# Kernel tuning notes

Measured on AMD Instinct MI355X. Metric: run time of the kernel, lower is better.

## Reference

```python
import jax, jax.numpy as jnp
import numpy as np

N = 2708
IN_C = 1433
OUT_C = 64


def setup_inputs() -> dict:
    key = jax.random.key(0)
    k1, k2, k3, k4, k5, k6, k7 = jax.random.split(key, 7)
    X = jax.random.normal(k1, (N, IN_C), dtype=jnp.float32)
    A = jax.random.randint(k2, (N, N), 0, 2, dtype=jnp.int32)  # dense binary adjacency mask
    # Graph Fourier basis: orthonormal-ish random matrix (QR of gaussian)
    U = jnp.linalg.qr(jax.random.normal(k3, (N, N), dtype=jnp.float32))[0]
    s = 1.0 / np.sqrt(IN_C)
    W_K = jax.random.normal(k4, (OUT_C, IN_C), dtype=jnp.float32) * s
    W_Q = jax.random.normal(k5, (OUT_C, IN_C), dtype=jnp.float32) * s
    W_V = jax.random.normal(k6, (OUT_C, IN_C), dtype=jnp.float32) * s
    lmbd = jax.random.uniform(k7, (N, 1), dtype=jnp.float32)
    return {"X": X, "A": A, "U": U, "W_K": W_K, "W_Q": W_Q, "W_V": W_V, "lmbd": lmbd}


def reference(X, A, U, W_K, W_Q, W_V, lmbd):
    # Linear projections (torch nn.Linear: x @ W.T)
    K = X @ W_K.T  # [N, d]
    Q = X @ W_Q.T  # [N, d]
    V = X @ W_V.T  # [N, d]
    d_k = K.shape[-1]
    E = (Q @ K.T) / d_k  # [N, N]
    # spectral filtering: igft(lmbd * gft(E)) = U @ (lmbd * (U^T @ E))
    E = jnp.abs(U @ (lmbd * (U.T @ E)))
    # masked softmax over neighbors; dropout p=0 in eval mode (no-op)
    E_masked = jnp.where(A == 0, -jnp.inf, E)
    alpha = jax.nn.softmax(E_masked, axis=-1)
    H = alpha @ V  # [N, d]
    return H
```

## Files before the change

kernel.cpp:

```cpp
#include <hip/hip_runtime.h>

#define NV 2708
#define INC 1433
#define XCOLS 1472
#define UDIM 2752
#define PSTR 2728
#define BSTR 2752
#define SLAB ((size_t)(2752*64))
#define MWPR 88
#define NSP 8
#define NSU 22

typedef __attribute__((ext_vector_type(8))) short bf16x8;
typedef __attribute__((ext_vector_type(4))) float f32x4;
typedef __attribute__((ext_vector_type(4))) unsigned short u16x4;

__device__ __forceinline__ unsigned short f2bf(float f){
  union { float f; unsigned int i; } v; v.f = f;
  return (unsigned short)((v.i + 0x7fffu + ((v.i >> 16) & 1u)) >> 16);
}

__device__ __forceinline__ void conv_row(const float* __restrict__ src,
                                         unsigned short* __restrict__ dst, int tid){
  const int sh = ((unsigned int)((size_t)src >> 2)) & 1;
  if (tid == 0){ int ce = sh ? 0 : (INC - 1); dst[ce] = f2bf(src[ce]); }
  const float2* s2 = (const float2*)(src + sh);
  for (int c2 = tid; c2 < (INC - 1)/2; c2 += 256){
    float2 v = s2[c2];
    int c = sh + c2*2;
    dst[c]     = f2bf(v.x);
    dst[c + 1] = f2bf(v.y);
  }
  for (int c = INC + tid; c < XCOLS; c += 256) dst[c] = 0;
}

__global__ __launch_bounds__(256) void convert_all(
    const float* __restrict__ X, const float* __restrict__ WK,
    const float* __restrict__ WQ, const float* __restrict__ WV,
    const float* __restrict__ U, const int* __restrict__ A,
    unsigned short* __restrict__ Xbf, unsigned short* __restrict__ Wbf,
    unsigned short* __restrict__ Ubf, unsigned int* __restrict__ Abits)
{
  const int bx = blockIdx.x;
  const int tid = threadIdx.x;
  if (bx < 2752){
    const int row = bx;
    unsigned short* dst = Ubf + (size_t)row*UDIM;
    if (row < NV){
      const float* src = U + (size_t)row*NV;
      for (int c4 = tid; c4 < 688; c4 += 256){
        float4 v = make_float4(0.f,0.f,0.f,0.f);
        if (c4 < 677) v = *(const float4*)(src + c4*4);
        u16x4 h = { f2bf(v.x), f2bf(v.y), f2bf(v.z), f2bf(v.w) };
        *(u16x4*)(dst + c4*4) = h;
      }
    } else {
      u16x4 zz = {0,0,0,0};
      for (int c4 = tid; c4 < 688; c4 += 256) *(u16x4*)(dst + c4*4) = zz;
    }
  } else if (bx < 5504){
    const int row = bx - 2752;
    unsigned short* dst = Xbf + (size_t)row*XCOLS;
    if (row < NV){
      conv_row(X + (size_t)row*INC, dst, tid);
    } else {
      u16x4 zz = {0,0,0,0};
      for (int c4 = tid; c4 < XCOLS/4; c4 += 256) *(u16x4*)(dst + c4*4) = zz;
    }
  } else if (bx < 5696){
    const int row = bx - 5504;
    const float* s = (row < 64) ? WK : (row < 128) ? WQ : WV;
    conv_row(s + (size_t)(row & 63)*INC, Wbf + (size_t)row*XCOLS, tid);
  } else {
    const int i = bx - 5696;
    const int lane = tid & 63, wave = tid >> 6;
    const int* arow = A + (size_t)i*NV;
    unsigned int* drow = Abits + (size_t)i*MWPR;
    for (int g = wave; g < 11; g += 4){
      int base = g*256 + lane*4;
      int4 v = make_int4(0,0,0,0);
      if (base < NV) v = *(const int4*)(arow + base);
      unsigned long long m0 = __ballot(v.x != 0);
      unsigned long long m1 = __ballot(v.y != 0);
      unsigned long long m2 = __ballot(v.z != 0);
      unsigned long long m3 = __ballot(v.w != 0);
      if (lane < 8){
        unsigned long long mm = (lane < 2) ? m0 : (lane < 4) ? m1 : (lane < 6) ? m2 : m3;
        drow[g*8 + lane] = (lane & 1) ? (unsigned int)(mm >> 32) : (unsigned int)mm;
      }
    }
  }
}

__global__ __launch_bounds__(256) void proj(
    const unsigned short* __restrict__ Xbf, const unsigned short* __restrict__ Wbf,
    float* __restrict__ part)
{
  __shared__ __align__(16) unsigned short At[64*72];
  __shared__ __align__(16) unsigned short Bt[64*72];
  const int tid = threadIdx.x;
  const int lane = tid & 63, wave = tid >> 6, quad = lane >> 4, lr = lane & 15;
  const int m0 = blockIdx.x * 64;
  const int s  = blockIdx.y, z = blockIdx.z;
  const int kbeg = s * 192, kend = min(kbeg + 192, XCOLS);
  const int wm = (wave & 1) * 32, wn = (wave >> 1) * 32;
  const unsigned short* Wz = Wbf + (size_t)z*64*XCOLS;
  const int srow = wave*8 + (lane >> 3), seg = lane & 7;
  f32x4 acc[2][2] = {};

  for (int k0 = kbeg; k0 < kend; k0 += 64){
    #pragma unroll
    for (int e = 0; e < 2; e++){
      int row = e*32 + srow;
      bf16x8 xa = *(const bf16x8*)(Xbf + (size_t)(m0+row)*XCOLS + k0 + seg*8);
      bf16x8 wb = *(const bf16x8*)(Wz  + (size_t)row*XCOLS      + k0 + seg*8);
      *(bf16x8*)&At[row*72 + seg*8] = xa;
      *(bf16x8*)&Bt[row*72 + seg*8] = wb;
    }
    __syncthreads();
    #pragma unroll
    for (int ks = 0; ks < 2; ks++){
      bf16x8 af[2], bv[2];
      #pragma unroll
      for (int t = 0; t < 2; t++){
        af[t] = *(const bf16x8*)&At[(wm + t*16 + lr)*72 + ks*32 + quad*8];
        bv[t] = *(const bf16x8*)&Bt[(wn + t*16 + lr)*72 + ks*32 + quad*8];
      }
      #pragma unroll
      for (int tm = 0; tm < 2; tm++)
        #pragma unroll
        for (int tn = 0; tn < 2; tn++)
          acc[tm][tn] = __builtin_amdgcn_mfma_f32_16x16x32_bf16(af[tm], bv[tn], acc[tm][tn], 0, 0, 0);
    }
    __syncthreads();
  }
  float* dst = part + (size_t)(z*NSP + s) * SLAB;
  #pragma unroll
  for (int tm = 0; tm < 2; tm++)
    #pragma unroll
    for (int tn = 0; tn < 2; tn++)
      #pragma unroll
      for (int e = 0; e < 4; e++)
        dst[(size_t)(m0 + wm + tm*16 + quad*4 + e)*64 + wn + tn*16 + lr] = acc[tm][tn][e];
}

__global__ __launch_bounds__(256) void reduce_proj(
    const float* __restrict__ part, unsigned short* __restrict__ K16f,
    unsigned short* __restrict__ QT16, unsigned short* __restrict__ VTf)
{
  int idx = blockIdx.x*256 + threadIdx.x;
  int z = blockIdx.y;
  int m = idx >> 6, c = idx & 63;
  const float* base = part + (size_t)z*NSP*SLAB + idx;
  float v = 0.f;
  #pragma unroll
  for (int s = 0; s < NSP; s++) v += base[s*SLAB];
  unsigned short h = (m < NV) ? f2bf(v) : (unsigned short)0;
  if (z == 0){
    if (m < 2720) K16f[((m>>4)*2 + (c>>5))*512 + (m&15)*32 + (c&31)] = h;
  } else if (z == 1){
    QT16[(size_t)c*BSTR + m] = h;
  } else {
    if (m < 2720) VTf[(m>>5)*2048 + c*32 + (m&31)] = h;
  }
}

__global__ __launch_bounds__(256) void gemmG(
    const unsigned short* __restrict__ Ubf, const unsigned short* __restrict__ QT,
    float* __restrict__ part)
{
  __shared__ __align__(16) unsigned short At[64*72];
  __shared__ __align__(16) unsigned short Bt[64*72];
  const int tid = threadIdx.x;
  const int lane = tid & 63, wave = tid >> 6, quad = lane >> 4, lr = lane & 15;
  const int m0 = blockIdx.x * 64;
  const int s  = blockIdx.y;
  const int kbeg = s * 128, kend = min(kbeg + 128, UDIM);
  const int wm = (wave & 1) * 32, wn = (wave >> 1) * 32;
  const int bc = tid >> 2, bseg = tid & 3;
  const int ml = (lane & 15)*4, koff = wave*16 + (lane >> 4);
  f32x4 acc[2][2] = {};

  for (int k0 = kbeg; k0 < kend; k0 += 64){
    #pragma unroll
    for (int e = 0; e < 4; e++){
      int kl = koff + e*4;
      u16x4 v = *(const u16x4*)(Ubf + (size_t)(k0+kl)*UDIM + m0 + ml);
      At[(ml+0)*72 + kl] = v[0];
      At[(ml+1)*72 + kl] = v[1];
      At[(ml+2)*72 + kl] = v[2];
      At[(ml+3)*72 + kl] = v[3];
    }
    {
      const unsigned short* q = QT + (size_t)bc*BSTR + k0 + bseg*16;
      *(bf16x8*)&Bt[bc*72 + bseg*16]     = *(const bf16x8*)(q);
      *(bf16x8*)&Bt[bc*72 + bseg*16 + 8] = *(const bf16x8*)(q + 8);
    }
    __syncthreads();
    #pragma unroll
    for (int ks = 0; ks < 2; ks++){
      bf16x8 af[2], bv[2];
      #pragma unroll
      for (int t = 0; t < 2; t++){
        af[t] = *(const bf16x8*)&At[(wm + t*16 + lr)*72 + ks*32 + quad*8];
        bv[t] = *(const bf16x8*)&Bt[(wn + t*16 + lr)*72 + ks*32 + quad*8];
      }
      #pragma unroll
      for (int tm = 0; tm < 2; tm++)
        #pragma unroll
        for (int tn = 0; tn < 2; tn++)
          acc[tm][tn] = __builtin_amdgcn_mfma_f32_16x16x32_bf16(af[tm], bv[tn], acc[tm][tn], 0, 0, 0);
    }
    __syncthreads();
  }
  float* dst = part + (size_t)s * SLAB;
  #pragma unroll
  for (int tm = 0; tm < 2; tm++)
    #pragma unroll
    for (int tn = 0; tn < 2; tn++)
      #pragma unroll
      for (int e = 0; e < 4; e++)
        dst[(size_t)(m0 + wm + tm*16 + quad*4 + e)*64 + wn + tn*16 + lr] = acc[tm][tn][e];
}

__global__ __launch_bounds__(256) void reduce_g(
    const float* __restrict__ part, const float* __restrict__ lm,
    unsigned short* __restrict__ G2T)
{
  int idx = blockIdx.x*256 + threadIdx.x;
  int m = idx >> 6, c = idx & 63;
  const float* base = part + idx;
  float v = 0.f;
  #pragma unroll
  for (int s = 0; s < NSU; s++) v += base[s*SLAB];
  unsigned short h = 0;
  if (m < NV) h = f2bf(v * lm[m] * (1.0f/64.0f));
  G2T[(size_t)c*BSTR + m] = h;
}

__global__ __launch_bounds__(256) void gemmF(
    const unsigned short* __restrict__ Ubf, const unsigned short* __restrict__ G2T,
    float* __restrict__ part)
{
  __shared__ __align__(16) unsigned short At[64*72];
  __shared__ __align__(16) unsigned short Bt[64*72];
  const int tid = threadIdx.x;
  const int lane = tid & 63, wave = tid >> 6, quad = lane >> 4, lr = lane & 15;
  const int m0 = blockIdx.x * 64;
  const int s  = blockIdx.y;
  const int kbeg = s * 128, kend = min(kbeg + 128, UDIM);
  const int wm = (wave & 1) * 32, wn = (wave >> 1) * 32;
  const int bc = tid >> 2, bseg = tid & 3;
  const int srow = wave*8 + (lane >> 3), seg = lane & 7;
  f32x4 acc[2][2] = {};

  for (int k0 = kbeg; k0 < kend; k0 += 64){
    #pragma unroll
    for (int e = 0; e < 2; e++){
      int row = e*32 + srow;
      bf16x8 ua = *(const bf16x8*)(Ubf + (size_t)(m0+row)*UDIM + k0 + seg*8);
      *(bf16x8*)&At[row*72 + seg*8] = ua;
    }
    {
      const unsigned short* g = G2T + (size_t)bc*BSTR + k0 + bseg*16;
      *(bf16x8*)&Bt[bc*72 + bseg*16]     = *(const bf16x8*)(g);
      *(bf16x8*)&Bt[bc*72 + bseg*16 + 8] = *(const bf16x8*)(g + 8);
    }
    __syncthreads();
    #pragma unroll
    for (int ks = 0; ks < 2; ks++){
      bf16x8 af[2], bv[2];
      #pragma unroll
      for (int t = 0; t < 2; t++){
        af[t] = *(const bf16x8*)&At[(wm + t*16 + lr)*72 + ks*32 + quad*8];
        bv[t] = *(const bf16x8*)&Bt[(wn + t*16 + lr)*72 + ks*32 + quad*8];
      }
      #pragma unroll
      for (int tm = 0; tm < 2; tm++)
        #pragma unroll
        for (int tn = 0; tn < 2; tn++)
          acc[tm][tn] = __builtin_amdgcn_mfma_f32_16x16x32_bf16(af[tm], bv[tn], acc[tm][tn], 0, 0, 0);
    }
    __syncthreads();
  }
  float* dst = part + (size_t)s * SLAB;
  #pragma unroll
  for (int tm = 0; tm < 2; tm++)
    #pragma unroll
    for (int tn = 0; tn < 2; tn++)
      #pragma unroll
      for (int e = 0; e < 4; e++)
        dst[(size_t)(m0 + wm + tm*16 + quad*4 + e)*64 + wn + tn*16 + lr] = acc[tm][tn][e];
}

__global__ __launch_bounds__(512) void fused_attn(
    const float* __restrict__ partF, const unsigned short* __restrict__ K16f,
    const unsigned int* __restrict__ Abits, const unsigned short* __restrict__ VTf,
    float* __restrict__ Hout)
{
  __shared__ __align__(16) unsigned short pbuf[16*PSTR];
  __shared__ __align__(16) unsigned short fbuf[16*64];
  __shared__ unsigned int mrow[16*MWPR];
  __shared__ float swave[8][16];
  __shared__ float rinv[16];
  __shared__ __align__(16) float obuf[4][256];
  const int tid  = threadIdx.x;
  const int lane = tid & 63, wave = tid >> 6;
  const int quad = lane >> 4, lr = lane & 15;
  const int i0 = blockIdx.x * 16;

  #pragma unroll
  for (int h = 0; h < 2; h++){
    int idx = h*512 + tid;
    const float* base = partF + (size_t)(i0 + (idx >> 6))*64 + (idx & 63);
    float v = 0.f;
    #pragma unroll
    for (int s = 0; s < NSU; s++) v += base[s*SLAB];
    fbuf[idx] = f2bf(v);
  }
  for (int idx = tid; idx < 16*MWPR; idx += 512){
    int r = idx / MWPR;
    unsigned int v = 0;
    if (i0 + r < NV) v = Abits[(size_t)(i0 + r)*MWPR + (idx - r*MWPR)];
    mrow[idx] = v;
  }
  __syncthreads();

  const bf16x8 af0 = *(const bf16x8*)&fbuf[lr*64 + quad*8];
  const bf16x8 af1 = *(const bf16x8*)&fbuf[lr*64 + 32 + quad*8];
  float psum[4] = {0.f, 0.f, 0.f, 0.f};
  {
    int t = wave;
    const unsigned short* kb = K16f + t*1024 + lr*32 + quad*8;
    bf16x8 b0 = *(const bf16x8*)(kb);
    bf16x8 b1 = *(const bf16x8*)(kb + 512);
    while (t < 170){
      int tn = t + 8;
      bf16x8 n0 = b0, n1 = b1;
      if (tn < 170){
        const unsigned short* nb = K16f + tn*1024 + lr*32 + quad*8;
        n0 = *(const bf16x8*)(nb);
        n1 = *(const bf16x8*)(nb + 512);
      }
      f32x4 sv0 = {}, sv1 = {};
      sv0 = __builtin_amdgcn_mfma_f32_16x16x32_bf16(af0, b0, sv0, 0, 0, 0);
      sv1 = __builtin_amdgcn_mfma_f32_16x16x32_bf16(af1, b1, sv1, 0, 0, 0);
      f32x4 sv = sv0 + sv1;
      {
        int col = t*16 + lr;
        int ss = col & 255, ll = ss >> 2;
        int wsh = (col >> 8)*8 + (ss & 3)*2 + (ll >> 5);
        int bit = ll & 31;
        #pragma unroll
        for (int e = 0; e < 4; e++){
          int r = quad*4 + e;
          float p = 0.f;
          if ((mrow[r*MWPR + wsh] >> bit) & 1u) p = __expf(fabsf(sv[e]));
          psum[e] += p;
          pbuf[r*PSTR + col] = f2bf(p);
        }
      }
      b0 = n0; b1 = n1; t = tn;
    }
  }
  #pragma unroll
  for (int e = 0; e < 4; e++){
    float v = psum[e];
    #pragma unroll
    for (int o = 1; o <= 8; o <<= 1) v += __shfl_xor(v, o, 64);
    if (lr == 0) swave[wave][quad*4 + e] = v;
  }
  __syncthreads();
  if (tid < 16){
    float s = 0.f;
    #pragma unroll
    for (int w = 0; w < 8; w++) s += swave[w][tid];
    rinv[tid] = (s > 0.f) ? (1.f/s) : 0.f;
  }
  __syncthreads();

  const int c0 = (wave & 3) * 16;
  const int ktbeg = (wave >> 2) ? 43 : 0;
  const int ktend = (wave >> 2) ? 85 : 43;
  f32x4 acc = {};
  {
    bf16x8 bv = *(const bf16x8*)&VTf[ktbeg*2048 + (c0 + lr)*32 + quad*8];
    for (int kt = ktbeg; kt < ktend; kt++){
      bf16x8 bn = bv;
      if (kt + 1 < ktend) bn = *(const bf16x8*)&VTf[(kt+1)*2048 + (c0 + lr)*32 + quad*8];
      bf16x8 af = *(const bf16x8*)&pbuf[lr*PSTR + kt*32 + quad*8];
      acc = __builtin_amdgcn_mfma_f32_16x16x32_bf16(af, bv, acc, 0, 0, 0);
      bv = bn;
    }
  }
  if (wave >= 4) *(f32x4*)&obuf[wave & 3][lane*4] = acc;
  __syncthreads();
  if (wave < 4){
    f32x4 o = *(const f32x4*)&obuf[wave][lane*4];
    acc += o;
    #pragma unroll
    for (int e = 0; e < 4; e++){
      int r = quad*4 + e;
      int i = i0 + r;
      if (i < NV) Hout[(size_t)i*64 + c0 + lr] = acc[e] * rinv[r];
    }
  }
}

extern "C" void kernel_launch(void* const* d_in, const int* in_sizes, int n_in,
                              void* d_out, int out_size, void* d_ws, size_t ws_size,
                              hipStream_t stream){
  (void)in_sizes; (void)n_in; (void)out_size; (void)ws_size;
  const float* X  = (const float*)d_in[0];
  const int*   A  = (const int*)d_in[1];
  const float* U  = (const float*)d_in[2];
  const float* WK = (const float*)d_in[3];
  const float* WQ = (const float*)d_in[4];
  const float* WV = (const float*)d_in[5];
  const float* lm = (const float*)d_in[6];

  char* ws = (char*)d_ws;
  size_t off = 0;
  auto alloc = [&](size_t bytes){ size_t o = off; off = (off + bytes + 255) & ~(size_t)255; return o; };
  float*          part = (float*)(ws + alloc(24*SLAB*4));
  unsigned short* Ubf  = (unsigned short*)(ws + alloc((size_t)UDIM*UDIM*2));
  unsigned short* Xbf  = (unsigned short*)(ws + alloc((size_t)UDIM*XCOLS*2));
  unsigned short* Wbf  = (unsigned short*)(ws + alloc((size_t)192*XCOLS*2));
  unsigned short* K16f = (unsigned short*)(ws + alloc((size_t)170*1024*2));
  unsigned short* QT16 = (unsigned short*)(ws + alloc((size_t)64*BSTR*2));
  unsigned short* G2T  = (unsigned short*)(ws + alloc((size_t)64*BSTR*2));
  unsigned short* VTf  = (unsigned short*)(ws + alloc((size_t)85*2048*2));
  unsigned int*   Abits= (unsigned int*)(ws + alloc((size_t)NV*MWPR*4));

  convert_all<<<dim3(8404), 256, 0, stream>>>(X, WK, WQ, WV, U, A, Xbf, Wbf, Ubf, Abits);
  proj<<<dim3(43, NSP, 3), 256, 0, stream>>>(Xbf, Wbf, part);
  reduce_proj<<<dim3(688, 3), 256, 0, stream>>>(part, K16f, QT16, VTf);
  gemmG<<<dim3(43, NSU), 256, 0, stream>>>(Ubf, QT16, part);
  reduce_g<<<dim3(688), 256, 0, stream>>>(part, lm, G2T);
  gemmF<<<dim3(43, NSU), 256, 0, stream>>>(Ubf, G2T, part);
  fused_attn<<<dim3(170), 512, 0, stream>>>(part, K16f, Abits, VTf, (float*)d_out);
}
```

Measured before the change: 182.1 us.

## Replace split-K partial buffers and reduce kernels with atomic accumulation

```diff
diff --git a/kernel.cpp b/kernel.cpp
--- a/kernel.cpp
+++ b/kernel.cpp
@@ -6,10 +6,10 @@
 #define UDIM 2752
 #define PSTR 2728
 #define BSTR 2752
-#define SLAB ((size_t)(2752*64))
 #define MWPR 88
 #define NSP 8
 #define NSU 22
+#define ACCN 176128
 
 typedef __attribute__((ext_vector_type(8))) short bf16x8;
 typedef __attribute__((ext_vector_type(4))) float f32x4;
@@ -38,25 +38,34 @@
     const float* __restrict__ X, const float* __restrict__ WK,
     const float* __restrict__ WQ, const float* __restrict__ WV,
     const float* __restrict__ U, const int* __restrict__ A,
+    const float* __restrict__ lm,
     unsigned short* __restrict__ Xbf, unsigned short* __restrict__ Wbf,
-    unsigned short* __restrict__ Ubf, unsigned int* __restrict__ Abits)
+    unsigned short* __restrict__ Ubf, unsigned short* __restrict__ UbfL,
+    unsigned int* __restrict__ Abits, float* __restrict__ acc32)
 {
   const int bx = blockIdx.x;
   const int tid = threadIdx.x;
   if (bx < 2752){
     const int row = bx;
-    unsigned short* dst = Ubf + (size_t)row*UDIM;
+    unsigned short* dst  = Ubf  + (size_t)row*UDIM;
+    unsigned short* dstl = UbfL + (size_t)row*UDIM;
     if (row < NV){
       const float* src = U + (size_t)row*NV;
+      const float s = 1.0f/64.0f;
       for (int c4 = tid; c4 < 688; c4 += 256){
         float4 v = make_float4(0.f,0.f,0.f,0.f);
-        if (c4 < 677) v = *(const float4*)(src + c4*4);
-        u16x4 h = { f2bf(v.x), f2bf(v.y), f2bf(v.z), f2bf(v.w) };
-        *(u16x4*)(dst + c4*4) = h;
+        float4 l4 = make_float4(0.f,0.f,0.f,0.f);
+        if (c4 < 677){ v = *(const float4*)(src + c4*4); l4 = *(const float4*)(lm + c4*4); }
+        u16x4 h  = { f2bf(v.x), f2bf(v.y), f2bf(v.z), f2bf(v.w) };
+        u16x4 hl = { f2bf(v.x*l4.x*s), f2bf(v.y*l4.y*s), f2bf(v.z*l4.z*s), f2bf(v.w*l4.w*s) };
+        *(u16x4*)(dst  + c4*4) = h;
+        *(u16x4*)(dstl + c4*4) = hl;
       }
     } else {
       u16x4 zz = {0,0,0,0};
-      for (int c4 = tid; c4 < 688; c4 += 256) *(u16x4*)(dst + c4*4) = zz;
+      for (int c4 = tid; c4 < 688; c4 += 256){
+        *(u16x4*)(dst + c4*4) = zz; *(u16x4*)(dstl + c4*4) = zz;
+      }
     }
   } else if (bx < 5504){
     const int row = bx - 2752;
@@ -71,7 +80,7 @@
     const int row = bx - 5504;
     const float* s = (row < 64) ? WK : (row < 128) ? WQ : WV;
     conv_row(s + (size_t)(row & 63)*INC, Wbf + (size_t)row*XCOLS, tid);
-  } else {
+  } else if (bx < 8404){
     const int i = bx - 5696;
     const int lane = tid & 63, wave = tid >> 6;
     const int* arow = A + (size_t)i*NV;
@@ -89,12 +98,15 @@
         drow[g*8 + lane] = (lane & 1) ? (unsigned int)(mm >> 32) : (unsigned int)mm;
       }
     }
+  } else {
+    int idx = (bx - 8404)*256 + tid;
+    *(float4*)(acc32 + (size_t)idx*4) = make_float4(0.f,0.f,0.f,0.f);
   }
 }
 
 __global__ __launch_bounds__(256) void proj(
     const unsigned short* __restrict__ Xbf, const unsigned short* __restrict__ Wbf,
-    float* __restrict__ part)
+    float* __restrict__ K32, float* __restrict__ Q32, float* __restrict__ V32)
 {
   __shared__ __align__(16) unsigned short At[64*72];
   __shared__ __align__(16) unsigned short Bt[64*72];
@@ -134,40 +146,30 @@
     }
     __syncthreads();
   }
-  float* dst = part + (size_t)(z*NSP + s) * SLAB;
   #pragma unroll
   for (int tm = 0; tm < 2; tm++)
     #pragma unroll
     for (int tn = 0; tn < 2; tn++)
       #pragma unroll
-      for (int e = 0; e < 4; e++)
-        dst[(size_t)(m0 + wm + tm*16 + quad*4 + e)*64 + wn + tn*16 + lr] = acc[tm][tn][e];
-}
-
-__global__ __launch_bounds__(256) void reduce_proj(
-    const float* __restrict__ part, unsigned short* __restrict__ K16f,
-    unsigned short* __restrict__ QT16, unsigned short* __restrict__ VTf)
-{
-  int idx = blockIdx.x*256 + threadIdx.x;
-  int z = blockIdx.y;
-  int m = idx >> 6, c = idx & 63;
-  const float* base = part + (size_t)z*NSP*SLAB + idx;
-  float v = 0.f;
-  #pragma unroll
-  for (int s = 0; s < NSP; s++) v += base[s*SLAB];
-  unsigned short h = (m < NV) ? f2bf(v) : (unsigned short)0;
-  if (z == 0){
-    if (m < 2720) K16f[((m>>4)*2 + (c>>5))*512 + (m&15)*32 + (c&31)] = h;
-  } else if (z == 1){
-    QT16[(size_t)c*BSTR + m] = h;
-  } else {
-    if (m < 2720) VTf[(m>>5)*2048 + c*32 + (m&31)] = h;
-  }
+      for (int e = 0; e < 4; e++){
+        int m = m0 + wm + tm*16 + quad*4 + e;
+        int c = wn + tn*16 + lr;
+        float v = acc[tm][tn][e];
+        if (z == 0){
+          if (m < 2720) atomicAdd(&K32[((m>>4)*2 + (c>>5))*512 + (m&15)*32 + (c&31)], v);
+        } else if (z == 1){
+          atomicAdd(&Q32[(size_t)c*BSTR + m], v);
+        } else {
+          if (m < 2720) atomicAdd(&V32[(m>>5)*2048 + c*32 + (m&31)], v);
+        }
+      }
 }
 
 __global__ __launch_bounds__(256) void gemmG(
-    const unsigned short* __restrict__ Ubf, const unsigned short* __restrict__ QT,
-    float* __restrict__ part)
+    const unsigned short* __restrict__ UbfL, const float* __restrict__ Q32,
+    float* __restrict__ G32,
+    const float* __restrict__ K32, const float* __restrict__ V32,
+    unsigned short* __restrict__ K16f, unsigned short* __restrict__ VTf)
 {
   __shared__ __align__(16) unsigned short At[64*72];
   __shared__ __align__(16) unsigned short Bt[64*72];
@@ -181,20 +183,38 @@
   const int ml = (lane & 15)*4, koff = wave*16 + (lane >> 4);
   f32x4 acc[2][2] = {};
 
+  {
+    int bid = blockIdx.y*43 + blockIdx.x;
+    for (int i = bid*256 + tid; i < 2*174080; i += 946*256){
+      if (i < 174080) K16f[i] = f2bf(K32[i]);
+      else            VTf[i - 174080] = f2bf(V32[i - 174080]);
+    }
+  }
+
   for (int k0 = kbeg; k0 < kend; k0 += 64){
     #pragma unroll
     for (int e = 0; e < 4; e++){
       int kl = koff + e*4;
-      u16x4 v = *(const u16x4*)(Ubf + (size_t)(k0+kl)*UDIM + m0 + ml);
+      u16x4 v = *(const u16x4*)(UbfL + (size_t)(k0+kl)*UDIM + m0 + ml);
       At[(ml+0)*72 + kl] = v[0];
       At[(ml+1)*72 + kl] = v[1];
       At[(ml+2)*72 + kl] = v[2];
       At[(ml+3)*72 + kl] = v[3];
     }
     {
-      const unsigned short* q = QT + (size_t)bc*BSTR + k0 + bseg*16;
-      *(bf16x8*)&Bt[bc*72 + bseg*16]     = *(const bf16x8*)(q);
-      *(bf16x8*)&Bt[bc*72 + bseg*16 + 8] = *(const bf16x8*)(q + 8);
+      const float* q = Q32 + (size_t)bc*BSTR + k0 + bseg*16;
+      float4 qa = *(const float4*)(q);
+      float4 qb = *(const float4*)(q + 4);
+      float4 qc = *(const float4*)(q + 8);
+      float4 qd = *(const float4*)(q + 12);
+      u16x4 h0 = { f2bf(qa.x), f2bf(qa.y), f2bf(qa.z), f2bf(qa.w) };
+      u16x4 h1 = { f2bf(qb.x), f2bf(qb.y), f2bf(qb.z), f2bf(qb.w) };
+      u16x4 h2 = { f2bf(qc.x), f2bf(qc.y), f2bf(qc.z), f2bf(qc.w) };
+      u16x4 h3 = { f2bf(qd.x), f2bf(qd.y), f2bf(qd.z), f2bf(qd.w) };
+      *(u16x4*)&Bt[bc*72 + bseg*16]      = h0;
+      *(u16x4*)&Bt[bc*72 + bseg*16 + 4]  = h1;
+      *(u16x4*)&Bt[bc*72 + bseg*16 + 8]  = h2;
+      *(u16x4*)&Bt[bc*72 + bseg*16 + 12] = h3;
     }
     __syncthreads();
     #pragma unroll
@@ -213,34 +233,21 @@
     }
     __syncthreads();
   }
-  float* dst = part + (size_t)s * SLAB;
   #pragma unroll
   for (int tm = 0; tm < 2; tm++)
     #pragma unroll
     for (int tn = 0; tn < 2; tn++)
       #pragma unroll
-      for (int e = 0; e < 4; e++)
-        dst[(size_t)(m0 + wm + tm*16 + quad*4 + e)*64 + wn + tn*16 + lr] = acc[tm][tn][e];
-}
-
-__global__ __launch_bounds__(256) void reduce_g(
-    const float* __restrict__ part, const float* __restrict__ lm,
-    unsigned short* __restrict__ G2T)
-{
-  int idx = blockIdx.x*256 + threadIdx.x;
-  int m = idx >> 6, c = idx & 63;
-  const float* base = part + idx;
-  float v = 0.f;
-  #pragma unroll
-  for (int s = 0; s < NSU; s++) v += base[s*SLAB];
-  unsigned short h = 0;
-  if (m < NV) h = f2bf(v * lm[m] * (1.0f/64.0f));
-  G2T[(size_t)c*BSTR + m] = h;
+      for (int e = 0; e < 4; e++){
+        int m = m0 + wm + tm*16 + quad*4 + e;
+        int c = wn + tn*16 + lr;
+        atomicAdd(&G32[(size_t)c*BSTR + m], acc[tm][tn][e]);
+      }
 }
 
 __global__ __launch_bounds__(256) void gemmF(
-    const unsigned short* __restrict__ Ubf, const unsigned short* __restrict__ G2T,
-    float* __restrict__ part)
+    const unsigned short* __restrict__ Ubf, const float* __restrict__ G32,
+    float* __restrict__ F32)
 {
   __shared__ __align__(16) unsigned short At[64*72];
   __shared__ __align__(16) unsigned short Bt[64*72];
@@ -262,9 +269,19 @@
       *(bf16x8*)&At[row*72 + seg*8] = ua;
     }
     {
-      const unsigned short* g = G2T + (size_t)bc*BSTR + k0 + bseg*16;
-      *(bf16x8*)&Bt[bc*72 + bseg*16]     = *(const bf16x8*)(g);
-      *(bf16x8*)&Bt[bc*72 + bseg*16 + 8] = *(const bf16x8*)(g + 8);
+      const float* g = G32 + (size_t)bc*BSTR + k0 + bseg*16;
+      float4 qa = *(const float4*)(g);
+      float4 qb = *(const float4*)(g + 4);
+      float4 qc = *(const float4*)(g + 8);
+      float4 qd = *(const float4*)(g + 12);
+      u16x4 h0 = { f2bf(qa.x), f2bf(qa.y), f2bf(qa.z), f2bf(qa.w) };
+      u16x4 h1 = { f2bf(qb.x), f2bf(qb.y), f2bf(qb.z), f2bf(qb.w) };
+      u16x4 h2 = { f2bf(qc.x), f2bf(qc.y), f2bf(qc.z), f2bf(qc.w) };
+      u16x4 h3 = { f2bf(qd.x), f2bf(qd.y), f2bf(qd.z), f2bf(qd.w) };
+      *(u16x4*)&Bt[bc*72 + bseg*16]      = h0;
+      *(u16x4*)&Bt[bc*72 + bseg*16 + 4]  = h1;
+      *(u16x4*)&Bt[bc*72 + bseg*16 + 8]  = h2;
+      *(u16x4*)&Bt[bc*72 + bseg*16 + 12] = h3;
     }
     __syncthreads();
     #pragma unroll
@@ -283,18 +300,20 @@
     }
     __syncthreads();
   }
-  float* dst = part + (size_t)s * SLAB;
   #pragma unroll
   for (int tm = 0; tm < 2; tm++)
     #pragma unroll
     for (int tn = 0; tn < 2; tn++)
       #pragma unroll
-      for (int e = 0; e < 4; e++)
-        dst[(size_t)(m0 + wm + tm*16 + quad*4 + e)*64 + wn + tn*16 + lr] = acc[tm][tn][e];
+      for (int e = 0; e < 4; e++){
+        int m = m0 + wm + tm*16 + quad*4 + e;
+        int c = wn + tn*16 + lr;
+        atomicAdd(&F32[(size_t)m*64 + c], acc[tm][tn][e]);
+      }
 }
 
 __global__ __launch_bounds__(512) void fused_attn(
-    const float* __restrict__ partF, const unsigned short* __restrict__ K16f,
+    const float* __restrict__ F32, const unsigned short* __restrict__ K16f,
     const unsigned int* __restrict__ Abits, const unsigned short* __restrict__ VTf,
     float* __restrict__ Hout)
 {
@@ -309,15 +328,8 @@
   const int quad = lane >> 4, lr = lane & 15;
   const int i0 = blockIdx.x * 16;
 
-  #pragma unroll
-  for (int h = 0; h < 2; h++){
-    int idx = h*512 + tid;
-    const float* base = partF + (size_t)(i0 + (idx >> 6))*64 + (idx & 63);
-    float v = 0.f;
-    #pragma unroll
-    for (int s = 0; s < NSU; s++) v += base[s*SLAB];
-    fbuf[idx] = f2bf(v);
-  }
+  for (int idx = tid; idx < 1024; idx += 512)
+    fbuf[idx] = f2bf(F32[(size_t)(i0 + (idx >> 6))*64 + (idx & 63)]);
   for (int idx = tid; idx < 16*MWPR; idx += 512){
     int r = idx / MWPR;
     unsigned int v = 0;
@@ -422,21 +434,24 @@
   char* ws = (char*)d_ws;
   size_t off = 0;
   auto alloc = [&](size_t bytes){ size_t o = off; off = (off + bytes + 255) & ~(size_t)255; return o; };
-  float*          part = (float*)(ws + alloc(24*SLAB*4));
-  unsigned short* Ubf  = (unsigned short*)(ws + alloc((size_t)UDIM*UDIM*2));
-  unsigned short* Xbf  = (unsigned short*)(ws + alloc((size_t)UDIM*XCOLS*2));
-  unsigned short* Wbf  = (unsigned short*)(ws + alloc((size_t)192*XCOLS*2));
-  unsigned short* K16f = (unsigned short*)(ws + alloc((size_t)170*1024*2));
-  unsigned short* QT16 = (unsigned short*)(ws + alloc((size_t)64*BSTR*2));
-  unsigned short* G2T  = (unsigned short*)(ws + alloc((size_t)64*BSTR*2));
-  unsigned short* VTf  = (unsigned short*)(ws + alloc((size_t)85*2048*2));
-  unsigned int*   Abits= (unsigned int*)(ws + alloc((size_t)NV*MWPR*4));
-
-  convert_all<<<dim3(8404), 256, 0, stream>>>(X, WK, WQ, WV, U, A, Xbf, Wbf, Ubf, Abits);
-  proj<<<dim3(43, NSP, 3), 256, 0, stream>>>(Xbf, Wbf, part);
-  reduce_proj<<<dim3(688, 3), 256, 0, stream>>>(part, K16f, QT16, VTf);
-  gemmG<<<dim3(43, NSU), 256, 0, stream>>>(Ubf, QT16, part);
-  reduce_g<<<dim3(688), 256, 0, stream>>>(part, lm, G2T);
-  gemmF<<<dim3(43, NSU), 256, 0, stream>>>(Ubf, G2T, part);
-  fused_attn<<<dim3(170), 512, 0, stream>>>(part, K16f, Abits, VTf, (float*)d_out);
-}
+  float*          acc32 = (float*)(ws + alloc((size_t)5*ACCN*4));
+  unsigned short* Ubf   = (unsigned short*)(ws + alloc((size_t)UDIM*UDIM*2));
+  unsigned short* UbfL  = (unsigned short*)(ws + alloc((size_t)UDIM*UDIM*2));
+  unsigned short* Xbf   = (unsigned short*)(ws + alloc((size_t)UDIM*XCOLS*2));
+  unsigned short* Wbf   = (unsigned short*)(ws + alloc((size_t)192*XCOLS*2));
+  unsigned short* K16f  = (unsigned short*)(ws + alloc((size_t)170*1024*2));
+  unsigned short* VTf   = (unsigned short*)(ws + alloc((size_t)85*2048*2));
+  unsigned int*   Abits = (unsigned int*)(ws + alloc((size_t)NV*MWPR*4));
+  float* K32 = acc32;
+  float* Q32 = acc32 + ACCN;
+  float* V32 = acc32 + 2*ACCN;
+  float* G32 = acc32 + 3*ACCN;
+  float* F32 = acc32 + 4*ACCN;
+
+  convert_all<<<dim3(9264), 256, 0, stream>>>(X, WK, WQ, WV, U, A, lm,
+                                              Xbf, Wbf, Ubf, UbfL, Abits, acc32);
+  proj<<<dim3(43, NSP, 3), 256, 0, stream>>>(Xbf, Wbf, K32, Q32, V32);
+  gemmG<<<dim3(43, NSU), 256, 0, stream>>>(UbfL, Q32, G32, K32, V32, K16f, VTf);
+  gemmF<<<dim3(43, NSU), 256, 0, stream>>>(Ubf, G32, F32);
+  fused_attn<<<dim3(170), 512, 0, stream>>>(F32, K16f, Abits, VTf, (float*)d_out);
+}
```

After: 253.1 us. 38.9% more time.

## Pre-transpose U in convert pass and unify spectral GEMMs with 32-row tiles

Applied to the files above, without the earlier changes.

```diff
diff --git a/kernel.cpp b/kernel.cpp
--- a/kernel.cpp
+++ b/kernel.cpp
@@ -9,7 +9,7 @@
 #define SLAB ((size_t)(2752*64))
 #define MWPR 88
 #define NSP 8
-#define NSU 22
+#define NSU 11
 
 typedef __attribute__((ext_vector_type(8))) short bf16x8;
 typedef __attribute__((ext_vector_type(4))) float f32x4;
@@ -39,8 +39,10 @@
     const float* __restrict__ WQ, const float* __restrict__ WV,
     const float* __restrict__ U, const int* __restrict__ A,
     unsigned short* __restrict__ Xbf, unsigned short* __restrict__ Wbf,
-    unsigned short* __restrict__ Ubf, unsigned int* __restrict__ Abits)
-{
+    unsigned short* __restrict__ Ubf, unsigned short* __restrict__ UTbf,
+    unsigned int* __restrict__ Abits)
+{
+  __shared__ __align__(16) float tpose[64][68];
   const int bx = blockIdx.x;
   const int tid = threadIdx.x;
   if (bx < 2752){
@@ -71,7 +73,7 @@
     const int row = bx - 5504;
     const float* s = (row < 64) ? WK : (row < 128) ? WQ : WV;
     conv_row(s + (size_t)(row & 63)*INC, Wbf + (size_t)row*XCOLS, tid);
-  } else {
+  } else if (bx < 8404){
     const int i = bx - 5696;
     const int lane = tid & 63, wave = tid >> 6;
     const int* arow = A + (size_t)i*NV;
@@ -89,6 +91,28 @@
         drow[g*8 + lane] = (lane & 1) ? (unsigned int)(mm >> 32) : (unsigned int)mm;
       }
     }
+  } else {
+    const int t = bx - 8404;
+    const int tx = t % 43, ty = t / 43;
+    const int r0 = ty*64, c0 = tx*64;
+    #pragma unroll
+    for (int j = 0; j < 4; j++){
+      int row = j*16 + (tid >> 4);
+      int c4  = (tid & 15)*4;
+      float4 v = make_float4(0.f,0.f,0.f,0.f);
+      if (r0 + row < NV && c0 + c4 < NV)
+        v = *(const float4*)(U + (size_t)(r0+row)*NV + c0 + c4);
+      *(float4*)&tpose[row][c4] = v;
+    }
+    __syncthreads();
+    const int i = tid >> 2;
+    #pragma unroll
+    for (int j = 0; j < 4; j++){
+      int kk = ((tid & 3) + j*4)*4;
+      u16x4 h = { f2bf(tpose[kk+0][i]), f2bf(tpose[kk+1][i]),
+                  f2bf(tpose[kk+2][i]), f2bf(tpose[kk+3][i]) };
+      *(u16x4*)(UTbf + (size_t)(c0+i)*UDIM + r0 + kk) = h;
+    }
   }
 }
 
@@ -165,62 +189,50 @@
   }
 }
 
-__global__ __launch_bounds__(256) void gemmG(
-    const unsigned short* __restrict__ Ubf, const unsigned short* __restrict__ QT,
+__global__ __launch_bounds__(256) void gemmU(
+    const unsigned short* __restrict__ Arow, const unsigned short* __restrict__ Bcm,
     float* __restrict__ part)
 {
-  __shared__ __align__(16) unsigned short At[64*72];
+  __shared__ __align__(16) unsigned short At[32*72];
   __shared__ __align__(16) unsigned short Bt[64*72];
   const int tid = threadIdx.x;
   const int lane = tid & 63, wave = tid >> 6, quad = lane >> 4, lr = lane & 15;
-  const int m0 = blockIdx.x * 64;
+  const int m0 = blockIdx.x * 32;
   const int s  = blockIdx.y;
-  const int kbeg = s * 128, kend = min(kbeg + 128, UDIM);
-  const int wm = (wave & 1) * 32, wn = (wave >> 1) * 32;
+  const int kbeg = s * 256, kend = min(kbeg + 256, UDIM);
+  const int wm = (wave & 1) * 16, wn = (wave >> 1) * 32;
+  const int arow = tid >> 3, aseg = tid & 7;
   const int bc = tid >> 2, bseg = tid & 3;
-  const int ml = (lane & 15)*4, koff = wave*16 + (lane >> 4);
-  f32x4 acc[2][2] = {};
+  f32x4 acc[2] = {};
 
   for (int k0 = kbeg; k0 < kend; k0 += 64){
-    #pragma unroll
-    for (int e = 0; e < 4; e++){
-      int kl = koff + e*4;
-      u16x4 v = *(const u16x4*)(Ubf + (size_t)(k0+kl)*UDIM + m0 + ml);
-      At[(ml+0)*72 + kl] = v[0];
-      At[(ml+1)*72 + kl] = v[1];
-      At[(ml+2)*72 + kl] = v[2];
-      At[(ml+3)*72 + kl] = v[3];
-    }
+    *(bf16x8*)&At[arow*72 + aseg*8] =
+        *(const bf16x8*)(Arow + (size_t)(m0+arow)*UDIM + k0 + aseg*8);
     {
-      const unsigned short* q = QT + (size_t)bc*BSTR + k0 + bseg*16;
-      *(bf16x8*)&Bt[bc*72 + bseg*16]     = *(const bf16x8*)(q);
-      *(bf16x8*)&Bt[bc*72 + bseg*16 + 8] = *(const bf16x8*)(q + 8);
+      const unsigned short* b = Bcm + (size_t)bc*BSTR + k0 + bseg*16;
+      *(bf16x8*)&Bt[bc*72 + bseg*16]     = *(const bf16x8*)(b);
+      *(bf16x8*)&Bt[bc*72 + bseg*16 + 8] = *(const bf16x8*)(b + 8);
     }
     __syncthreads();
     #pragma unroll
     for (int ks = 0; ks < 2; ks++){
-      bf16x8 af[2], bv[2];
+      bf16x8 af = *(const bf16x8*)&At[(wm + lr)*72 + ks*32 + quad*8];
+      bf16x8 bv[2];
       #pragma unroll
-      for (int t = 0; t < 2; t++){
-        af[t] = *(const bf16x8*)&At[(wm + t*16 + lr)*72 + ks*32 + quad*8];
+      for (int t = 0; t < 2; t++)
         bv[t] = *(const bf16x8*)&Bt[(wn + t*16 + lr)*72 + ks*32 + quad*8];
-      }
       #pragma unroll
-      for (int tm = 0; tm < 2; tm++)
-        #pragma unroll
-        for (int tn = 0; tn < 2; tn++)
-          acc[tm][tn] = __builtin_amdgcn_mfma_f32_16x16x32_bf16(af[tm], bv[tn], acc[tm][tn], 0, 0, 0);
+      for (int t = 0; t < 2; t++)
+        acc[t] = __builtin_amdgcn_mfma_f32_16x16x32_bf16(af, bv[t], acc[t], 0, 0, 0);
     }
     __syncthreads();
   }
   float* dst = part + (size_t)s * SLAB;
   #pragma unroll
-  for (int tm = 0; tm < 2; tm++)
-    #pragma unroll
-    for (int tn = 0; tn < 2; tn++)
-      #pragma unroll
-      for (int e = 0; e < 4; e++)
-        dst[(size_t)(m0 + wm + tm*16 + quad*4 + e)*64 + wn + tn*16 + lr] = acc[tm][tn][e];
+  for (int t = 0; t < 2; t++)
+    #pragma unroll
+    for (int e = 0; e < 4; e++)
+      dst[(size_t)(m0 + wm + quad*4 + e)*64 + wn + t*16 + lr] = acc[t][e];
 }
 
 __global__ __launch_bounds__(256) void reduce_g(
@@ -236,61 +248,6 @@
   unsigned short h = 0;
   if (m < NV) h = f2bf(v * lm[m] * (1.0f/64.0f));
   G2T[(size_t)c*BSTR + m] = h;
-}
-
-__global__ __launch_bounds__(256) void gemmF(
-    const unsigned short* __restrict__ Ubf, const unsigned short* __restrict__ G2T,
-    float* __restrict__ part)
-{
-  __shared__ __align__(16) unsigned short At[64*72];
-  __shared__ __align__(16) unsigned short Bt[64*72];
-  const int tid = threadIdx.x;
-  const int lane = tid & 63, wave = tid >> 6, quad = lane >> 4, lr = lane & 15;
-  const int m0 = blockIdx.x * 64;
-  const int s  = blockIdx.y;
-  const int kbeg = s * 128, kend = min(kbeg + 128, UDIM);
-  const int wm = (wave & 1) * 32, wn = (wave >> 1) * 32;
-  const int bc = tid >> 2, bseg = tid & 3;
-  const int srow = wave*8 + (lane >> 3), seg = lane & 7;
-  f32x4 acc[2][2] = {};
-
-  for (int k0 = kbeg; k0 < kend; k0 += 64){
-    #pragma unroll
-    for (int e = 0; e < 2; e++){
-      int row = e*32 + srow;
-      bf16x8 ua = *(const bf16x8*)(Ubf + (size_t)(m0+row)*UDIM + k0 + seg*8);
-      *(bf16x8*)&At[row*72 + seg*8] = ua;
-    }
-    {
-      const unsigned short* g = G2T + (size_t)bc*BSTR + k0 + bseg*16;
-      *(bf16x8*)&Bt[bc*72 + bseg*16]     = *(const bf16x8*)(g);
-      *(bf16x8*)&Bt[bc*72 + bseg*16 + 8] = *(const bf16x8*)(g + 8);
-    }
-    __syncthreads();
-    #pragma unroll
-    for (int ks = 0; ks < 2; ks++){
-      bf16x8 af[2], bv[2];
-      #pragma unroll
-      for (int t = 0; t < 2; t++){
-        af[t] = *(const bf16x8*)&At[(wm + t*16 + lr)*72 + ks*32 + quad*8];
-        bv[t] = *(const bf16x8*)&Bt[(wn + t*16 + lr)*72 + ks*32 + quad*8];
-      }
-      #pragma unroll
-      for (int tm = 0; tm < 2; tm++)
-        #pragma unroll
-        for (int tn = 0; tn < 2; tn++)
-          acc[tm][tn] = __builtin_amdgcn_mfma_f32_16x16x32_bf16(af[tm], bv[tn], acc[tm][tn], 0, 0, 0);
-    }
-    __syncthreads();
-  }
-  float* dst = part + (size_t)s * SLAB;
-  #pragma unroll
-  for (int tm = 0; tm < 2; tm++)
-    #pragma unroll
-    for (int tn = 0; tn < 2; tn++)
-      #pragma unroll
-      for (int e = 0; e < 4; e++)
-        dst[(size_t)(m0 + wm + tm*16 + quad*4 + e)*64 + wn + tn*16 + lr] = acc[tm][tn][e];
 }
 
 __global__ __launch_bounds__(512) void fused_attn(
@@ -424,6 +381,7 @@
   auto alloc = [&](size_t bytes){ size_t o = off; off = (off + bytes + 255) & ~(size_t)255; return o; };
   float*          part = (float*)(ws + alloc(24*SLAB*4));
   unsigned short* Ubf  = (unsigned short*)(ws + alloc((size_t)UDIM*UDIM*2));
+  unsigned short* UTbf = (unsigned short*)(ws + alloc((size_t)UDIM*UDIM*2));
   unsigned short* Xbf  = (unsigned short*)(ws + alloc((size_t)UDIM*XCOLS*2));
   unsigned short* Wbf  = (unsigned short*)(ws + alloc((size_t)192*XCOLS*2));
   unsigned short* K16f = (unsigned short*)(ws + alloc((size_t)170*1024*2));
@@ -432,11 +390,12 @@
   unsigned short* VTf  = (unsigned short*)(ws + alloc((size_t)85*2048*2));
   unsigned int*   Abits= (unsigned int*)(ws + alloc((size_t)NV*MWPR*4));
 
-  convert_all<<<dim3(8404), 256, 0, stream>>>(X, WK, WQ, WV, U, A, Xbf, Wbf, Ubf, Abits);
+  convert_all<<<dim3(10253), 256, 0, stream>>>(X, WK, WQ, WV, U, A,
+                                               Xbf, Wbf, Ubf, UTbf, Abits);
   proj<<<dim3(43, NSP, 3), 256, 0, stream>>>(Xbf, Wbf, part);
   reduce_proj<<<dim3(688, 3), 256, 0, stream>>>(part, K16f, QT16, VTf);
-  gemmG<<<dim3(43, NSU), 256, 0, stream>>>(Ubf, QT16, part);
+  gemmU<<<dim3(86, NSU), 256, 0, stream>>>(UTbf, QT16, part);
   reduce_g<<<dim3(688), 256, 0, stream>>>(part, lm, G2T);
-  gemmF<<<dim3(43, NSU), 256, 0, stream>>>(Ubf, G2T, part);
+  gemmU<<<dim3(86, NSU), 256, 0, stream>>>(Ubf, G2T, part);
   fused_attn<<<dim3(170), 512, 0, stream>>>(part, K16f, Abits, VTf, (float*)d_out);
 }
```

Result: faster. 177.0 us (-2.8%).
